# Optimization experiments

Hardware: AMD Instinct MI355X
Metric: run time of the kernel (lower is better)

Reference implementation:

```python
import jax, jax.numpy as jnp
import numpy as np

N_NEIGHBORS = 16
N_CLASSES = 10

def setup_inputs() -> dict:
    key = jax.random.key(0)
    k1, k2, k3 = jax.random.split(key, 3)
    x = jax.random.normal(k1, (1024, 64), dtype=jnp.float32)
    train_data = jax.random.normal(k2, (100000, 64), dtype=jnp.float32)
    train_labels = jax.random.randint(k3, (100000,), 0, N_CLASSES, dtype=jnp.int64)
    return {"x": x, "train_data": train_data, "train_labels": train_labels}

def reference(x, train_data, train_labels):
    # Pairwise L2 distances [B, N] via the quadratic expansion (same math as cdist p=2)
    x2 = jnp.sum(x * x, axis=-1, keepdims=True)            # [B, 1]
    t2 = jnp.sum(train_data * train_data, axis=-1)          # [N]
    d2 = x2 - 2.0 * (x @ train_data.T) + t2                 # [B, N]
    dist = jnp.sqrt(jnp.maximum(d2, 0.0))
    # k smallest distances
    neg_d, idx = jax.lax.top_k(-dist, N_NEIGHBORS)           # [B, k]
    d = -neg_d
    labels = train_labels[idx]                               # [B, k] gather
    # weights = 'distance': inverse distance, with exact-match rows handled
    w = 1.0 / d
    inf_mask = jnp.isinf(w)
    inf_row = jnp.any(inf_mask, axis=1, keepdims=True)
    w = jnp.where(inf_row, inf_mask.astype(w.dtype), w)
    # scatter_add weighted votes into [B, C]
    B = x.shape[0]
    rows = jnp.arange(B)[:, None]
    proba = jnp.zeros((B, N_CLASSES), dtype=w.dtype).at[rows, labels].add(w)
    s = jnp.sum(proba, axis=1, keepdims=True)
    s = jnp.where(s == 0.0, jnp.float32(1.0), s)
    proba = proba / s
    return jnp.argmax(proba, axis=1), proba
```

## Files before the change

### kernel.cpp

```cpp
#include <hip/hip_runtime.h>
#include <math.h>


constexpr int D        = 64;
constexpr int K        = 16;
constexpr int NCLS     = 10;
constexpr int CHUNKLEN = 1024;
constexpr int NCHUNK   = 104;
constexpr int NPAD     = NCHUNK * 1024 + 64;
constexpr int NSUB     = 64;
constexpr int SUBLEN   = 128;
constexpr int SLOT     = 16;
constexpr int MSEL     = 48;
constexpr int SGPTS    = 16;
constexpr int SGBYTES  = SGPTS * 128;
constexpr int SLOTB    = SGBYTES + 256;
constexpr int NCVT     = (NPAD * 4) / 256;

typedef __attribute__((ext_vector_type(8))) short bf16x8_t;
typedef __attribute__((ext_vector_type(4))) float f32x4_t;
typedef unsigned short ushort_t;

__device__ __forceinline__ ushort_t f32_to_bf16_rne(float f) {
  unsigned int u = __float_as_uint(f);
  unsigned int r = u + 0x7FFFu + ((u >> 16) & 1u);
  return (ushort_t)(r >> 16);
}

__device__ __forceinline__ bf16x8_t pack_bf16x8(float4 a, float4 b) {
  union { ushort_t u[8]; bf16x8_t v; } r;
  r.u[0] = f32_to_bf16_rne(a.x); r.u[1] = f32_to_bf16_rne(a.y);
  r.u[2] = f32_to_bf16_rne(a.z); r.u[3] = f32_to_bf16_rne(a.w);
  r.u[4] = f32_to_bf16_rne(b.x); r.u[5] = f32_to_bf16_rne(b.y);
  r.u[6] = f32_to_bf16_rne(b.z); r.u[7] = f32_to_bf16_rne(b.w);
  return r.v;
}

__device__ __forceinline__ void glds16(const void* g, void* l) {
  __builtin_amdgcn_global_load_lds(
      (const __attribute__((address_space(1))) void*)g,
      (__attribute__((address_space(3))) void*)l, 16, 0, 0);
}
__device__ __forceinline__ void glds4(const void* g, void* l) {
  __builtin_amdgcn_global_load_lds(
      (const __attribute__((address_space(1))) void*)g,
      (__attribute__((address_space(3))) void*)l, 4, 0, 0);
}

__global__ __launch_bounds__(256) void knn_prep(
    const float* __restrict__ train, const float* __restrict__ x,
    ushort_t* __restrict__ tb, float* __restrict__ t2,
    float* __restrict__ nt2h, float* __restrict__ samp, int N)
{
  __shared__ float nh_l[4][16];
  const int tid = threadIdx.x;

  if ((int)blockIdx.x < NCVT) {
    int gid = blockIdx.x * 256 + tid;
    int row = gid >> 2, qt = gid & 3;
    ushort_t* dst = tb + (size_t)row * D + qt * 16;
    if (row >= N) {
      uint2 z = make_uint2(0u, 0u);
      #pragma unroll
      for (int i = 0; i < 4; ++i) *reinterpret_cast<uint2*>(dst + i * 4) = z;
      if (qt == 0) { t2[row] = INFINITY; nt2h[row] = -INFINITY; }
      return;
    }
    const float* src = train + (size_t)row * D + qt * 16;
    float nrm = 0.f;
    #pragma unroll
    for (int i = 0; i < 4; ++i) {
      float4 v = *reinterpret_cast<const float4*>(src + i * 4);
      nrm = fmaf(v.x, v.x, nrm); nrm = fmaf(v.y, v.y, nrm);
      nrm = fmaf(v.z, v.z, nrm); nrm = fmaf(v.w, v.w, nrm);
      uint2 hh = make_uint2(
        (unsigned)f32_to_bf16_rne(v.x) | ((unsigned)f32_to_bf16_rne(v.y) << 16),
        (unsigned)f32_to_bf16_rne(v.z) | ((unsigned)f32_to_bf16_rne(v.w) << 16));
      *reinterpret_cast<uint2*>(dst + i * 4) = hh;
    }
    nrm += __shfl_xor(nrm, 1);
    nrm += __shfl_xor(nrm, 2);
    if (qt == 0) { t2[row] = nrm; nt2h[row] = -0.5f * nrm; }
    return;
  }

  const int bid2 = blockIdx.x - NCVT;
  const int w = tid >> 6, lane = tid & 63;
  const int lh = lane & 15, lg = lane >> 4;
  const int qb = bid2 & 15, sub = bid2 >> 4;
  const int q = qb * 64 + w * 16 + lh;

  const float* xrp = x + (size_t)q * D + lg * 8;
  bf16x8_t B0 = pack_bf16x8(*reinterpret_cast<const float4*>(xrp),
                            *reinterpret_cast<const float4*>(xrp + 4));
  bf16x8_t B1 = pack_bf16x8(*reinterpret_cast<const float4*>(xrp + 32),
                            *reinterpret_cast<const float4*>(xrp + 36));

  float Ld[4] = {-INFINITY, -INFINITY, -INFINITY, -INFINITY};
  const int pstart = sub * SUBLEN;

  for (int j = 0; j < SUBLEN / 16; ++j) {
    const float* tr = train + (size_t)(pstart + j * 16 + lh) * D;
    float4 f0 = *reinterpret_cast<const float4*>(tr + lg * 8);
    float4 f1 = *reinterpret_cast<const float4*>(tr + lg * 8 + 4);
    float4 f2 = *reinterpret_cast<const float4*>(tr + 32 + lg * 8);
    float4 f3 = *reinterpret_cast<const float4*>(tr + 32 + lg * 8 + 4);
    bf16x8_t A0 = pack_bf16x8(f0, f1);
    bf16x8_t A1 = pack_bf16x8(f2, f3);
    float pn = 0.f;
    pn = fmaf(f0.x, f0.x, pn); pn = fmaf(f0.y, f0.y, pn);
    pn = fmaf(f0.z, f0.z, pn); pn = fmaf(f0.w, f0.w, pn);
    pn = fmaf(f1.x, f1.x, pn); pn = fmaf(f1.y, f1.y, pn);
    pn = fmaf(f1.z, f1.z, pn); pn = fmaf(f1.w, f1.w, pn);
    pn = fmaf(f2.x, f2.x, pn); pn = fmaf(f2.y, f2.y, pn);
    pn = fmaf(f2.z, f2.z, pn); pn = fmaf(f2.w, f2.w, pn);
    pn = fmaf(f3.x, f3.x, pn); pn = fmaf(f3.y, f3.y, pn);
    pn = fmaf(f3.z, f3.z, pn); pn = fmaf(f3.w, f3.w, pn);
    pn += __shfl_xor(pn, 16);
    pn += __shfl_xor(pn, 32);
    if (lg == 0) nh_l[w][lh] = -0.5f * pn;
    float4 nh = *reinterpret_cast<const float4*>(&nh_l[w][lg * 4]);
    f32x4_t c = {nh.x, nh.y, nh.z, nh.w};
    c = __builtin_amdgcn_mfma_f32_16x16x32_bf16(A0, B0, c, 0, 0, 0);
    c = __builtin_amdgcn_mfma_f32_16x16x32_bf16(A1, B1, c, 0, 0, 0);
    #pragma unroll
    for (int r = 0; r < 4; ++r) {
      float sv = c[r];
      if (sv > Ld[3]) {
        Ld[3] = sv;
        if (Ld[3] > Ld[2]) { float s_ = Ld[3]; Ld[3] = Ld[2]; Ld[2] = s_; }
        if (Ld[2] > Ld[1]) { float s_ = Ld[2]; Ld[2] = Ld[1]; Ld[1] = s_; }
        if (Ld[1] > Ld[0]) { float s_ = Ld[1]; Ld[1] = Ld[0]; Ld[0] = s_; }
      }
    }
  }

  float* outp = samp + (size_t)q * (NSUB * 16) + sub * 16 + lg * 4;
  *reinterpret_cast<float4*>(outp) = make_float4(Ld[0], Ld[1], Ld[2], Ld[3]);
}

__global__ __launch_bounds__(256) void knn_theta(
    const float* __restrict__ samp, float* __restrict__ theta, int B)
{
  const int w = threadIdx.x >> 6, lane = threadIdx.x & 63;
  const int q = blockIdx.x * 4 + w;
  if (q >= B) return;

  const float* s = samp + (size_t)q * (NSUB * 16) + lane * 16;
  float4 p0 = *reinterpret_cast<const float4*>(s);
  float4 p1 = *reinterpret_cast<const float4*>(s + 4);
  float4 p2 = *reinterpret_cast<const float4*>(s + 8);
  float4 p3 = *reinterpret_cast<const float4*>(s + 12);
  float L0[4] = {p0.x, p0.y, p0.z, p0.w};
  float L1[4] = {p1.x, p1.y, p1.z, p1.w};
  float L2[4] = {p2.x, p2.y, p2.z, p2.w};
  float L3[4] = {p3.x, p3.y, p3.z, p3.w};

  float th = -INFINITY;
  for (int r = 0; r < K; ++r) {
    float bd = fmaxf(fmaxf(L0[0], L1[0]), fmaxf(L2[0], L3[0]));
    #pragma unroll
    for (int sdx = 0; sdx < 6; ++sdx) bd = fmaxf(bd, __shfl_xor(bd, 32 >> sdx));
    if (L0[0] == bd) { L0[0] = L0[1]; L0[1] = L0[2]; L0[2] = L0[3]; L0[3] = -INFINITY; }
    if (L1[0] == bd) { L1[0] = L1[1]; L1[1] = L1[2]; L1[2] = L1[3]; L1[3] = -INFINITY; }
    if (L2[0] == bd) { L2[0] = L2[1]; L2[1] = L2[2]; L2[2] = L2[3]; L2[3] = -INFINITY; }
    if (L3[0] == bd) { L3[0] = L3[1]; L3[1] = L3[2]; L3[2] = L3[3]; L3[3] = -INFINITY; }
    th = bd;
  }
  if (lane == 0) theta[q] = th;
}

__global__ __launch_bounds__(256) void knn_filter(
    const ushort_t* __restrict__ tb, const float* __restrict__ x,
    const float* __restrict__ nt2h, const float* __restrict__ theta,
    int* __restrict__ cnts, int2* __restrict__ cand2)
{
  __shared__ char ring[4][3][SLOTB];
  __shared__ int  cnt_l[64];
  __shared__ int2 list_p[64][SLOT];

  const int tid = threadIdx.x;
  const int w = tid >> 6, lane = tid & 63;
  const int lh = lane & 15, lg = lane >> 4;

  const int d   = blockIdx.x + 16 * blockIdx.y;
  const int xcd = d & 7;
  const int t_  = d >> 3;
  const int qb  = t_ & 15;
  const int ch  = ((t_ >> 4) << 3) | xcd;

  const int q0  = qb * 64;
  const int wp0 = ch * CHUNKLEN + w * 256;

  if (tid < 64) cnt_l[tid] = 0;
  __syncthreads();

  bf16x8_t Bq0[4], Bq1[4];
  float th[4];
  #pragma unroll
  for (int ct = 0; ct < 4; ++ct) {
    const float* xrp = x + (size_t)(q0 + ct * 16 + lh) * D + lg * 8;
    Bq0[ct] = pack_bf16x8(*reinterpret_cast<const float4*>(xrp),
                          *reinterpret_cast<const float4*>(xrp + 4));
    Bq1[ct] = pack_bf16x8(*reinterpret_cast<const float4*>(xrp + 32),
                          *reinterpret_cast<const float4*>(xrp + 36));
    th[ct] = theta[q0 + ct * 16 + lh];
  }

  char* myring = &ring[w][0][0];
  const char*  gA = (const char*)(tb + (size_t)wp0 * D);
  const float* gN = nt2h + wp0;
  const int rowoff = (lane >> 3) * 128;
  const int swz    = (((lane & 7) ^ (lane >> 3)) << 4);
  const int lhx    = lh & 7;

  #define ISSUE(SG)                                                              \
    {                                                                            \
      char* sb = myring + ((SG) % 3) * SLOTB;                                    \
      const char* ga = gA + (size_t)(SG) * SGBYTES;                              \
      glds16(ga + rowoff + swz,        sb);                                      \
      glds16(ga + 1024 + rowoff + swz, sb + 1024);                               \
      glds4 (gN + (SG) * SGPTS + lane, sb + 2048);                               \
    }

  #define COMPUTE(SG)                                                            \
    {                                                                            \
      const char* sb = myring + ((SG) % 3) * SLOTB;                              \
      bf16x8_t A0 = *reinterpret_cast<const bf16x8_t*>(                          \
          sb + lh * 128 + ((lg ^ lhx) << 4));                                    \
      bf16x8_t A1 = *reinterpret_cast<const bf16x8_t*>(                          \
          sb + lh * 128 + (((lg + 4) ^ lhx) << 4));                              \
      float4 nh = *reinterpret_cast<const float4*>(sb + 2048 + lg * 16);         \
      const int pg = wp0 + (SG) * SGPTS + lg * 4;                                \
      _Pragma("unroll")                                                          \
      for (int ct = 0; ct < 4; ++ct) {                                           \
        f32x4_t c = {nh.x, nh.y, nh.z, nh.w};                                    \
        c = __builtin_amdgcn_mfma_f32_16x16x32_bf16(A0, Bq0[ct], c, 0, 0, 0);    \
        c = __builtin_amdgcn_mfma_f32_16x16x32_bf16(A1, Bq1[ct], c, 0, 0, 0);    \
        float mx = fmaxf(fmaxf(c[0], c[1]), fmaxf(c[2], c[3]));                  \
        if (mx >= th[ct]) {                                                      \
          const int qloc = ct * 16 + lh;                                         \
          _Pragma("unroll")                                                      \
          for (int r = 0; r < 4; ++r) {                                          \
            if (c[r] >= th[ct]) {                                                \
              int pos = atomicAdd(&cnt_l[qloc], 1);                              \
              if (pos < SLOT)                                                    \
                list_p[qloc][pos] = make_int2(pg + r, __float_as_int(c[r]));     \
            }                                                                    \
          }                                                                      \
        }                                                                        \
      }                                                                          \
    }

  asm volatile("s_waitcnt vmcnt(0)" ::: "memory");
  ISSUE(0);
  ISSUE(1);
  #pragma unroll
  for (int it = 0; it < 16; ++it) {
    if (it < 14) {
      ISSUE(it + 2);
      asm volatile("s_waitcnt vmcnt(6)" ::: "memory");
    } else if (it == 14) {
      asm volatile("s_waitcnt vmcnt(3)" ::: "memory");
    } else {
      asm volatile("s_waitcnt vmcnt(0)" ::: "memory");
    }
    COMPUTE(it);
  }
  #undef ISSUE
  #undef COMPUTE

  __syncthreads();
  if (tid < 64) {
    int n = cnt_l[tid]; if (n > SLOT) n = SLOT;
    size_t o = (size_t)(q0 + tid) * NCHUNK + ch;
    cnts[o] = n;
    for (int j = 0; j < n; ++j) cand2[o * SLOT + j] = list_p[tid][j];
  }
}

__global__ __launch_bounds__(256) void knn_vote(
    const float* __restrict__ x, const float* __restrict__ train,
    const float* __restrict__ t2, const int* __restrict__ labels,
    const int* __restrict__ cnts, const int2* __restrict__ cand2,
    float* __restrict__ out, int B, int N)
{
  __shared__ int2  cpair[NCHUNK * SLOT + 4];
  __shared__ float sortd[MSEL];
  __shared__ int   sorti[MSEL];
  __shared__ float xs[D];
  __shared__ int   total_s;
  __shared__ float x2_s;

  const int tid = threadIdx.x;
  const int w = tid >> 6, lane = tid & 63;
  const int q = blockIdx.x;

  if (tid == 0) total_s = 0;
  if (tid < D) xs[tid] = x[(size_t)q * D + tid];
  if (tid < MSEL) { sortd[tid] = INFINITY; sorti[tid] = 0x7fffffff; }
  __syncthreads();

  if (w == 0) {
    float v = xs[lane];
    float s = v * v;
    #pragma unroll
    for (int o = 32; o > 0; o >>= 1) s += __shfl_xor(s, o);
    if (lane == 0) x2_s = s;
  }
  if (tid < NCHUNK) {
    int n = cnts[(size_t)q * NCHUNK + tid];
    int base = atomicAdd(&total_s, n);
    const int2* src = cand2 + ((size_t)q * NCHUNK + tid) * SLOT;
    for (int j = 0; j < n; ++j) cpair[base + j] = src[j];
  }
  __syncthreads();

  const int total = total_s;
  const int totalPad = (total + 3) & ~3;
  const float x2 = x2_s;
  if (tid < totalPad - total)
    cpair[total + tid] = make_int2(0x7fffffff, __float_as_int(-INFINITY));
  __syncthreads();

  for (int j = tid; j < total; j += 256) {
    int2 mine = cpair[j];
    float ms = __int_as_float(mine.y);
    int   mi = mine.x;
    int rank = 0;
    for (int k = 0; k < totalPad; k += 4) {
      int2 o0 = cpair[k];     int2 o1 = cpair[k + 1];
      int2 o2 = cpair[k + 2]; int2 o3 = cpair[k + 3];
      float s0 = __int_as_float(o0.y), s1 = __int_as_float(o1.y);
      float s2 = __int_as_float(o2.y), s3 = __int_as_float(o3.y);
      rank += ((s0 > ms || (s0 == ms && o0.x < mi)) ? 1 : 0)
            + ((s1 > ms || (s1 == ms && o1.x < mi)) ? 1 : 0)
            + ((s2 > ms || (s2 == ms && o2.x < mi)) ? 1 : 0)
            + ((s3 > ms || (s3 == ms && o3.x < mi)) ? 1 : 0);
    }
    if (rank < MSEL) { sortd[rank] = ms; sorti[rank] = mi; }
  }
  __syncthreads();

  if (tid < MSEL * 4) {
    const int ci = tid >> 2, qt = tid & 3;
    const int idx = sorti[ci];
    float dot = 0.f;
    if (idx != 0x7fffffff) {
      const float* tr = train + (size_t)idx * D + qt * 16;
      #pragma unroll
      for (int i = 0; i < 4; ++i) {
        float4 tv = *reinterpret_cast<const float4*>(tr + i * 4);
        dot = fmaf(xs[qt * 16 + i * 4 + 0], tv.x, dot);
        dot = fmaf(xs[qt * 16 + i * 4 + 1], tv.y, dot);
        dot = fmaf(xs[qt * 16 + i * 4 + 2], tv.z, dot);
        dot = fmaf(xs[qt * 16 + i * 4 + 3], tv.w, dot);
      }
    }
    dot += __shfl_xor(dot, 1);
    dot += __shfl_xor(dot, 2);
    if (qt == 0)
      sortd[ci] = (idx != 0x7fffffff)
                ? fmaxf(x2 - 2.f * dot + t2[idx], 0.f) : INFINITY;
  }
  __syncthreads();

  if (w == 0) {
    float vd = (lane < MSEL) ? sortd[lane] : INFINITY;
    int   vi = (lane < MSEL) ? sorti[lane] : 0x7fffffff;
    float myD = INFINITY; int myI = 0;
    for (int r = 0; r < K; ++r) {
      float bd = vd; int bi = vi;
      #pragma unroll
      for (int s = 0; s < 6; ++s) {
        int off = 32 >> s;
        float od = __shfl_xor(bd, off);
        int   oi = __shfl_xor(bi, off);
        if (od < bd || (od == bd && oi < bi)) { bd = od; bi = oi; }
      }
      if (vd == bd && vi == bi) { vd = INFINITY; vi = 0x7fffffff; }
      if (lane == r) { myD = bd; myI = bi; }
    }

    int valid = (lane < K) && (myD < INFINITY) && (myI < N);
    float dist = sqrtf(fmaxf(myD, 0.f));
    int lab = labels[(valid && myI < N) ? myI : 0];
    int isz = (valid && dist == 0.f) ? 1 : 0;
    float wgt = 1.f / dist;

    float accw[NCLS]; float acci[NCLS]; int anyInf = 0;
    #pragma unroll
    for (int c = 0; c < NCLS; ++c) { accw[c] = 0.f; acci[c] = 0.f; }
    for (int r = 0; r < K; ++r) {
      int   vr   = __shfl(valid, r);
      int   labr = __shfl(lab, r);
      float wgtr = __shfl(wgt, r);
      int   iszr = __shfl(isz, r);
      if (vr) {
        anyInf |= iszr;
        #pragma unroll
        for (int c = 0; c < NCLS; ++c) {
          accw[c] += (labr == c) ? wgtr : 0.f;
          acci[c] += (labr == c && iszr) ? 1.f : 0.f;
        }
      }
    }

    if (lane == 0) {
      float proba[NCLS]; float s = 0.f;
      #pragma unroll
      for (int c = 0; c < NCLS; ++c) { proba[c] = anyInf ? acci[c] : accw[c]; s += proba[c]; }
      if (s == 0.f) s = 1.f;
      #pragma unroll
      for (int c = 0; c < NCLS; ++c) proba[c] = proba[c] / s;
      int best = 0; float bv = proba[0];
      #pragma unroll
      for (int c = 1; c < NCLS; ++c) if (proba[c] > bv) { bv = proba[c]; best = c; }
      out[q] = (float)best;
      #pragma unroll
      for (int c = 0; c < NCLS; ++c) out[B + q * NCLS + c] = proba[c];
    }
  }
}

extern "C" void kernel_launch(void* const* d_in, const int* in_sizes, int n_in,
                              void* d_out, int out_size, void* d_ws, size_t ws_size,
                              hipStream_t stream)
{
  const float* x      = (const float*)d_in[0];
  const float* train  = (const float*)d_in[1];
  const int*   labels = (const int*)d_in[2];
  float* out = (float*)d_out;

  const int B = in_sizes[0] / D;
  const int N = in_sizes[2];

  char* ws = (char*)d_ws;
  size_t off = 0;
  ushort_t* train_bf = (ushort_t*)(ws + off); off += (size_t)NPAD * D * 2;
  float*    t2       = (float*)(ws + off);    off += (size_t)NPAD * 4;
  float*    nt2h     = (float*)(ws + off);    off += (size_t)NPAD * 4;
  float*    theta    = (float*)(ws + off);    off += (size_t)B * 4;
  int*      cnts     = (int*)(ws + off);      off += (size_t)B * NCHUNK * 4;
  int2*     cand2    = (int2*)(ws + off);     off += (size_t)B * NCHUNK * SLOT * 8;
  float*    samp     = (float*)cand2;

  knn_prep<<<NCVT + (B / 64) * NSUB, 256, 0, stream>>>(train, x, train_bf, t2, nt2h, samp, N);
  knn_theta<<<(B + 3) / 4, 256, 0, stream>>>(samp, theta, B);
  knn_filter<<<dim3(16, NCHUNK), 256, 0, stream>>>(train_bf, x, nt2h, theta, cnts, cand2);
  knn_vote<<<B, 256, 0, stream>>>(x, train, t2, labels, cnts, cand2, out, B, N);
}
```

Measured before the change: 100.3 us.

## Enlarge filter chunks and fold theta selection into prep via last-block counter

The filter kernel's train chunks grow from 1024 to 1664 points, which cuts the grid from 104 to 64 chunk columns, and the per-query candidate slots grow to 23. Fewer chunks means less candidate output and less merge work in the vote stage. The separate theta kernel is removed: the last prep block to finish for each query block, found with an atomic counter, computes the thresholds. This saves one launch, but adds a memset, serial tail work in 16 blocks, and atomic/fence overhead.

Result: slower. 182.3 us (+81.8%).

```diff
diff --git a/kernel.cpp b/kernel.cpp
--- a/kernel.cpp
+++ b/kernel.cpp
@@ -5,16 +5,17 @@
 constexpr int D        = 64;
 constexpr int K        = 16;
 constexpr int NCLS     = 10;
-constexpr int CHUNKLEN = 1024;
-constexpr int NCHUNK   = 104;
-constexpr int NPAD     = NCHUNK * 1024 + 64;
+constexpr int CHUNKLEN = 1664;
+constexpr int NCHUNK   = 64;
+constexpr int NPAD     = NCHUNK * CHUNKLEN + 64;
 constexpr int NSUB     = 64;
 constexpr int SUBLEN   = 128;
-constexpr int SLOT     = 16;
+constexpr int SLOT     = 23;
 constexpr int MSEL     = 48;
 constexpr int SGPTS    = 16;
 constexpr int SGBYTES  = SGPTS * 128;
 constexpr int SLOTB    = SGBYTES + 256;
+constexpr int NSG      = CHUNKLEN / 4 / SGPTS;
 constexpr int NCVT     = (NPAD * 4) / 256;
 
 typedef __attribute__((ext_vector_type(8))) short bf16x8_t;
@@ -50,9 +51,11 @@
 __global__ __launch_bounds__(256) void knn_prep(
     const float* __restrict__ train, const float* __restrict__ x,
     ushort_t* __restrict__ tb, float* __restrict__ t2,
-    float* __restrict__ nt2h, float* __restrict__ samp, int N)
+    float* __restrict__ nt2h, float* __restrict__ samp,
+    int* __restrict__ done, float* __restrict__ theta, int N)
 {
   __shared__ float nh_l[4][16];
+  __shared__ int lastFlag;
   const int tid = threadIdx.x;
 
   if ((int)blockIdx.x < NCVT) {
@@ -137,37 +140,41 @@
 
   float* outp = samp + (size_t)q * (NSUB * 16) + sub * 16 + lg * 4;
   *reinterpret_cast<float4*>(outp) = make_float4(Ld[0], Ld[1], Ld[2], Ld[3]);
-}
-
-__global__ __launch_bounds__(256) void knn_theta(
-    const float* __restrict__ samp, float* __restrict__ theta, int B)
-{
-  const int w = threadIdx.x >> 6, lane = threadIdx.x & 63;
-  const int q = blockIdx.x * 4 + w;
-  if (q >= B) return;
-
-  const float* s = samp + (size_t)q * (NSUB * 16) + lane * 16;
-  float4 p0 = *reinterpret_cast<const float4*>(s);
-  float4 p1 = *reinterpret_cast<const float4*>(s + 4);
-  float4 p2 = *reinterpret_cast<const float4*>(s + 8);
-  float4 p3 = *reinterpret_cast<const float4*>(s + 12);
-  float L0[4] = {p0.x, p0.y, p0.z, p0.w};
-  float L1[4] = {p1.x, p1.y, p1.z, p1.w};
-  float L2[4] = {p2.x, p2.y, p2.z, p2.w};
-  float L3[4] = {p3.x, p3.y, p3.z, p3.w};
-
-  float th = -INFINITY;
-  for (int r = 0; r < K; ++r) {
-    float bd = fmaxf(fmaxf(L0[0], L1[0]), fmaxf(L2[0], L3[0]));
-    #pragma unroll
-    for (int sdx = 0; sdx < 6; ++sdx) bd = fmaxf(bd, __shfl_xor(bd, 32 >> sdx));
-    if (L0[0] == bd) { L0[0] = L0[1]; L0[1] = L0[2]; L0[2] = L0[3]; L0[3] = -INFINITY; }
-    if (L1[0] == bd) { L1[0] = L1[1]; L1[1] = L1[2]; L1[2] = L1[3]; L1[3] = -INFINITY; }
-    if (L2[0] == bd) { L2[0] = L2[1]; L2[1] = L2[2]; L2[2] = L2[3]; L2[3] = -INFINITY; }
-    if (L3[0] == bd) { L3[0] = L3[1]; L3[1] = L3[2]; L3[2] = L3[3]; L3[3] = -INFINITY; }
-    th = bd;
-  }
-  if (lane == 0) theta[q] = th;
+
+  __syncthreads();
+  if (tid == 0) {
+    __threadfence();
+    int old = atomicAdd(&done[qb], 1);
+    lastFlag = (old == 63);
+  }
+  __syncthreads();
+  if (lastFlag) {
+    __threadfence();
+    for (int i = 0; i < 16; ++i) {
+      const int qq = qb * 64 + w * 16 + i;
+      const float* s = samp + (size_t)qq * (NSUB * 16) + lane * 16;
+      float4 p0 = *reinterpret_cast<const float4*>(s);
+      float4 p1 = *reinterpret_cast<const float4*>(s + 4);
+      float4 p2 = *reinterpret_cast<const float4*>(s + 8);
+      float4 p3 = *reinterpret_cast<const float4*>(s + 12);
+      float L0[4] = {p0.x, p0.y, p0.z, p0.w};
+      float L1[4] = {p1.x, p1.y, p1.z, p1.w};
+      float L2[4] = {p2.x, p2.y, p2.z, p2.w};
+      float L3[4] = {p3.x, p3.y, p3.z, p3.w};
+      float th = -INFINITY;
+      for (int r = 0; r < K; ++r) {
+        float bd = fmaxf(fmaxf(L0[0], L1[0]), fmaxf(L2[0], L3[0]));
+        #pragma unroll
+        for (int sdx = 0; sdx < 6; ++sdx) bd = fmaxf(bd, __shfl_xor(bd, 32 >> sdx));
+        if (L0[0] == bd) { L0[0] = L0[1]; L0[1] = L0[2]; L0[2] = L0[3]; L0[3] = -INFINITY; }
+        if (L1[0] == bd) { L1[0] = L1[1]; L1[1] = L1[2]; L1[2] = L1[3]; L1[3] = -INFINITY; }
+        if (L2[0] == bd) { L2[0] = L2[1]; L2[1] = L2[2]; L2[2] = L2[3]; L2[3] = -INFINITY; }
+        if (L3[0] == bd) { L3[0] = L3[1]; L3[1] = L3[2]; L3[2] = L3[3]; L3[3] = -INFINITY; }
+        th = bd;
+      }
+      if (lane == 0) theta[qq] = th;
+    }
+  }
 }
 
 __global__ __launch_bounds__(256) void knn_filter(
@@ -190,7 +197,7 @@
   const int ch  = ((t_ >> 4) << 3) | xcd;
 
   const int q0  = qb * 64;
-  const int wp0 = ch * CHUNKLEN + w * 256;
+  const int wp0 = ch * CHUNKLEN + w * (CHUNKLEN / 4);
 
   if (tid < 64) cnt_l[tid] = 0;
   __syncthreads();
@@ -256,11 +263,11 @@
   ISSUE(0);
   ISSUE(1);
   #pragma unroll
-  for (int it = 0; it < 16; ++it) {
-    if (it < 14) {
+  for (int it = 0; it < NSG; ++it) {
+    if (it < NSG - 2) {
       ISSUE(it + 2);
       asm volatile("s_waitcnt vmcnt(6)" ::: "memory");
-    } else if (it == 14) {
+    } else if (it == NSG - 2) {
       asm volatile("s_waitcnt vmcnt(3)" ::: "memory");
     } else {
       asm volatile("s_waitcnt vmcnt(0)" ::: "memory");
@@ -441,12 +448,14 @@
   float*    t2       = (float*)(ws + off);    off += (size_t)NPAD * 4;
   float*    nt2h     = (float*)(ws + off);    off += (size_t)NPAD * 4;
   float*    theta    = (float*)(ws + off);    off += (size_t)B * 4;
+  int*      done     = (int*)(ws + off);      off += 64;
   int*      cnts     = (int*)(ws + off);      off += (size_t)B * NCHUNK * 4;
   int2*     cand2    = (int2*)(ws + off);     off += (size_t)B * NCHUNK * SLOT * 8;
   float*    samp     = (float*)cand2;
 
-  knn_prep<<<NCVT + (B / 64) * NSUB, 256, 0, stream>>>(train, x, train_bf, t2, nt2h, samp, N);
-  knn_theta<<<(B + 3) / 4, 256, 0, stream>>>(samp, theta, B);
+  hipMemsetAsync(done, 0, 16 * sizeof(int), stream);
+  knn_prep<<<NCVT + (B / 64) * NSUB, 256, 0, stream>>>(
+      train, x, train_bf, t2, nt2h, samp, done, theta, N);
   knn_filter<<<dim3(16, NCHUNK), 256, 0, stream>>>(train_bf, x, nt2h, theta, cnts, cand2);
   knn_vote<<<B, 256, 0, stream>>>(x, train, t2, labels, cnts, cand2, out, B, N);
 }
```
